# Performance work log

Hardware: AMD Instinct MI355X
Metric: run time of the kernel (lower is better)

The kernel has to match this reference:

```python
import jax, jax.numpy as jnp
import numpy as np

S, D = 16384, 1024


def setup_inputs() -> dict:
    key = jax.random.key(0)
    ks = jax.random.split(key, 7)
    stdv = 1.0 / np.sqrt(D)
    u = lambda k, shape: jax.random.uniform(k, shape, jnp.float32, -stdv, stdv)
    return {
        "x": jax.random.normal(ks[0], (S, D), jnp.float32),
        "Wq": u(ks[1], (D, D)), "bq": u(ks[2], (D,)),
        "Wk": u(ks[3], (D, D)), "bk": u(ks[4], (D,)),
        "Wv": u(ks[5], (D, D)), "bv": u(ks[6], (D,)),
    }


def reference(x, Wq, bq, Wk, bk, Wv, bv):
    # torch.nn.Linear: y = x @ W^T + b
    q = x @ Wq.T + bq          # [S, D]
    k = x @ Wk.T + bk          # [S, D]
    v = x @ Wv.T + bv          # [S, D]
    d = x.shape[-1]
    # NOTE: faithful to source -- scores are over the FEATURE axis: [D, D]
    scores = jnp.einsum('sd,se->de', q, k) / jnp.sqrt(jnp.float32(d))
    attn = jax.nn.softmax(scores, axis=-1)   # [D, D]
    out = v @ attn                           # [S, D]
    return out, attn
```

## Files before the change

### kernel.cpp

```cpp
#include <hip/hip_runtime.h>
#include <hip/hip_bf16.h>
#include <stdint.h>


#define S_ 16384
#define D_ 1024

typedef _Float16 half8 __attribute__((ext_vector_type(8)));
typedef _Float16 half4 __attribute__((ext_vector_type(4)));
typedef float f32x4 __attribute__((ext_vector_type(4)));

__device__ __forceinline__ void gload_lds16(const _Float16* g, _Float16* l) {
    __builtin_amdgcn_global_load_lds(
        (const __attribute__((address_space(1))) void*)g,
        (__attribute__((address_space(3))) void*)l, 16, 0, 0);
}

#define VM8() do { asm volatile("s_waitcnt vmcnt(8)" ::: "memory"); __builtin_amdgcn_sched_barrier(0); } while (0)
#define VM0() do { asm volatile("s_waitcnt vmcnt(0)" ::: "memory"); __builtin_amdgcn_sched_barrier(0); } while (0)
#define BAR() __builtin_amdgcn_s_barrier()
#define LGKM0() do { asm volatile("s_waitcnt lgkmcnt(0)" ::: "memory"); __builtin_amdgcn_sched_barrier(0); } while (0)
#define LGKM8() do { asm volatile("s_waitcnt lgkmcnt(8)" ::: "memory"); __builtin_amdgcn_sched_barrier(0); } while (0)
#define PRIO1() __builtin_amdgcn_s_setprio(1)
#define PRIO0() __builtin_amdgcn_s_setprio(0)

#define STAGEA(H, KT, NX) do { \
    const _Float16* _s = srcA + (size_t)((H) * 128) * lda + (size_t)(KT) * 64; \
    _Float16* _d = AsS + (NX) * 16384 + ((H) * 128 + 8 * w) * 64; \
    gload_lds16(_s, _d); \
    gload_lds16(_s + (size_t)64 * lda, _d + 4096); \
} while (0)

#define STAGEB(H, KT, NX) do { \
    const _Float16* _s = srcB + (size_t)((H) * 128) * ldb + (size_t)(KT) * 64; \
    _Float16* _d = BsS + (NX) * 16384 + ((H) * 128 + 8 * w) * 64; \
    gload_lds16(_s, _d); \
    gload_lds16(_s + (size_t)64 * ldb, _d + 4096); \
} while (0)

#define READA(PA, QA) do { _Pragma("unroll") \
    for (int fm = 0; fm < 4; ++fm) { \
        af[fm][0] = *(const half8*)((PA) + (((QA) * 128 + fm * 16) << 7) + cx0); \
        af[fm][1] = *(const half8*)((PA) + (((QA) * 128 + fm * 16) << 7) + cx1); } \
} while (0)

#define READB(PB, BF, QB) do { _Pragma("unroll") \
    for (int fn = 0; fn < 2; ++fn) { \
        BF[fn][0] = *(const half8*)((PB) + (((QB) * 128 + fn * 16) << 7) + cx0); \
        BF[fn][1] = *(const half8*)((PB) + (((QB) * 128 + fn * 16) << 7) + cx1); } \
} while (0)

#define MFMAB(QA, QB, BF) do { _Pragma("unroll") \
    for (int fm = 0; fm < 4; ++fm) { _Pragma("unroll") \
        for (int fn = 0; fn < 2; ++fn) { \
            f32x4 _c = acc[(QA) * 4 + fm][(QB) * 2 + fn]; \
            _c = __builtin_amdgcn_mfma_f32_16x16x32_f16(af[fm][0], BF[fn][0], _c, 0, 0, 0); \
            _c = __builtin_amdgcn_mfma_f32_16x16x32_f16(af[fm][1], BF[fn][1], _c, 0, 0, 0); \
            acc[(QA) * 4 + fm][(QB) * 2 + fn] = _c; } } \
} while (0)

__global__ __launch_bounds__(512, 2)
void gemm256(const _Float16* __restrict__ A, const _Float16* __restrict__ B,
             _Float16* __restrict__ C,
             int lda, int ldb, int ldc, int ksub, long long mn,
             int ntx, int ntxy, int cpx) {
    __shared__ _Float16 SM2[65536];
    _Float16* AsS = SM2;
    _Float16* BsS = SM2 + 32768;
    const int t = threadIdx.x;
    const int l = t & 63;
    const int w = t >> 6;
    const int wm = w >> 2, wn = w & 3;

    const int hb = blockIdx.x;
    const int lg = (hb & 7) * cpx + (hb >> 3);
    const int bz = lg / ntxy;
    const int rem = lg - bz * ntxy;
    const int by = rem / ntx;
    const int bx = rem - by * ntx;
    const size_t m0 = (size_t)by * 256;
    const size_t n0 = (size_t)bx * 256;
    const size_t k0 = (size_t)bz * (size_t)ksub;
    const long long coff = (long long)bz * mn;

    const int colsw = 8 * ((l & 7) ^ (l >> 3));
    const _Float16* srcA = A + (m0 + 8 * w + (l >> 3)) * (size_t)lda + k0 + colsw;
    const _Float16* srcB = B + (n0 + 8 * w + (l >> 3)) * (size_t)ldb + k0 + colsw;

    const int cx0 = (((l >> 4) << 4)) ^ ((l & 7) << 4);
    const int cx1 = (64 + ((l >> 4) << 4)) ^ ((l & 7) << 4);
    const char* basePA = (const char*)AsS + ((wm * 64 + (l & 15)) << 7);
    const char* basePB = (const char*)BsS + ((wn * 32 + (l & 15)) << 7);

    f32x4 acc[8][4] = {};
    half8 af[4][2], bf0[2][2], bf1[2][2];

    const int nk = ksub >> 6;

    STAGEA(0, 0, 0); STAGEB(0, 0, 0); STAGEB(1, 0, 0); STAGEA(1, 0, 0);
    STAGEA(0, 1, 1); STAGEB(0, 1, 1); STAGEB(1, 1, 1); STAGEA(1, 1, 1);

    for (int kt = 0; kt < nk; ++kt) {
        const int p = kt & 1;
        const int ks = kt + 2;
        const bool hs = ks < nk;
        const char* pA = basePA + p * 32768;
        const char* pB = basePB + p * 32768;

        if (kt == nk - 1) VM0(); else VM8();
        BAR();

        READA(pA, 0); READB(pB, bf0, 0);
        LGKM8();
        BAR(); LGKM0();
        PRIO1(); MFMAB(0, 0, bf0); PRIO0(); BAR();

        READB(pB, bf1, 1);
        if (hs) { STAGEA(0, ks, p); STAGEB(0, ks, p); }
        BAR(); LGKM0();
        PRIO1(); MFMAB(0, 1, bf1); PRIO0(); BAR();

        READA(pA, 1);
        if (hs) STAGEB(1, ks, p);
        BAR(); LGKM0();
        PRIO1(); MFMAB(1, 1, bf1); PRIO0(); BAR();

        if (hs) STAGEA(1, ks, p);
        PRIO1(); MFMAB(1, 0, bf0); PRIO0(); BAR();
    }

    _Float16* eb = SM2;
    const int cr = (l >> 4) << 2;
    const int cc = l & 15;
#pragma unroll
    for (int h = 0; h < 2; ++h) {
        BAR();
#pragma unroll
        for (int mm = 0; mm < 4; ++mm) {
#pragma unroll
            for (int n = 0; n < 4; ++n) {
                const int lrow0 = wm * 64 + mm * 16 + cr;
                const int lcol = (n >> 1) * 128 + wn * 32 + (n & 1) * 16 + cc;
#pragma unroll
                for (int r = 0; r < 4; ++r)
                    eb[(lrow0 + r) * 264 + lcol] = (_Float16)acc[h * 4 + mm][n][r];
            }
        }
        LGKM0();
        BAR();
#pragma unroll
        for (int i = 0; i < 8; ++i) {
            const int lrow = w * 16 + i * 2 + (l >> 5);
            const half8 v = *(const half8*)(eb + lrow * 264 + (l & 31) * 8);
            const size_t row = m0 + (size_t)h * 128 + lrow;
            const size_t col = n0 + (l & 31) * 8;
            __builtin_nontemporal_store(v,
                (half8*)(C + coff + (long long)row * ldc + col));
        }
        LGKM0();
    }
}

#define STG128(SRC, LD, DST, KT) do { \
    const _Float16* _s = (SRC) + (size_t)(KT) * 64; \
    _Float16* _d = (DST) + 8 * w * 64; \
    gload_lds16(_s, _d); \
    gload_lds16(_s + (size_t)32 * (LD), _d + 2048); \
    gload_lds16(_s + (size_t)64 * (LD), _d + 4096); \
    gload_lds16(_s + (size_t)96 * (LD), _d + 6144); \
} while (0)

__global__ __launch_bounds__(256, 2)
void gemm128(const _Float16* __restrict__ A, const _Float16* __restrict__ B,
             float* __restrict__ C, const float* __restrict__ bias,
             int lda, int ldb, int ldc, int ksub,
             int ntx, int cpx) {
    __shared__ _Float16 SM[32768];
    const int t = threadIdx.x;
    const int l = t & 63;
    const int w = t >> 6;
    const int wm = w >> 1, wn = w & 1;

    const int hb = blockIdx.x;
    const int lg = (hb & 7) * cpx + (hb >> 3);
    const int by = lg / ntx;
    const int bx = lg - by * ntx;
    const size_t m0 = (size_t)by * 128;
    const size_t n0 = (size_t)bx * 128;

    const int colsw = 8 * ((l & 7) ^ (l >> 3));
    const _Float16* srcA = A + (m0 + 8 * w + (l >> 3)) * (size_t)lda + colsw;
    const _Float16* srcB = B + (n0 + 8 * w + (l >> 3)) * (size_t)ldb + colsw;

    const int cx0 = (((l >> 4) << 4)) ^ ((l & 7) << 4);
    const int cx1 = (64 + ((l >> 4) << 4)) ^ ((l & 7) << 4);
    const char* basePA = (const char*)SM + ((wm * 64 + (l & 15)) << 7);
    const char* basePB = (const char*)SM + 32768 + ((wn * 64 + (l & 15)) << 7);

    f32x4 acc[4][4] = {};
    half8 af[4][2], bf[4][2];

    const int nk = ksub >> 6;

    STG128(srcA, lda, SM + 0, 0);        STG128(srcB, ldb, SM + 16384, 0);
    STG128(srcA, lda, SM + 8192, 1);     STG128(srcB, ldb, SM + 24576, 1);

    for (int kt = 0; kt < nk; ++kt) {
        const int p = kt & 1;
        const int ks = kt + 2;
        const bool hs = ks < nk;
        const char* pA = basePA + p * 16384;
        const char* pB = basePB + p * 16384;

        if (kt == nk - 1) VM0(); else VM8();
        BAR();

#pragma unroll
        for (int fm = 0; fm < 4; ++fm) {
            af[fm][0] = *(const half8*)(pA + ((fm * 16) << 7) + cx0);
            af[fm][1] = *(const half8*)(pA + ((fm * 16) << 7) + cx1);
        }
#pragma unroll
        for (int fn = 0; fn < 4; ++fn) {
            bf[fn][0] = *(const half8*)(pB + ((fn * 16) << 7) + cx0);
            bf[fn][1] = *(const half8*)(pB + ((fn * 16) << 7) + cx1);
        }
        LGKM0();
        PRIO1();
#pragma unroll
        for (int fm = 0; fm < 4; ++fm)
#pragma unroll
            for (int fn = 0; fn < 4; ++fn)
                acc[fm][fn] = __builtin_amdgcn_mfma_f32_16x16x32_f16(af[fm][0], bf[fn][0], acc[fm][fn], 0, 0, 0);
        PRIO0();
        BAR();

        if (hs) {
            STG128(srcA, lda, SM + p * 8192, ks);
            STG128(srcB, ldb, SM + 16384 + p * 8192, ks);
        }
        PRIO1();
#pragma unroll
        for (int fm = 0; fm < 4; ++fm)
#pragma unroll
            for (int fn = 0; fn < 4; ++fn)
                acc[fm][fn] = __builtin_amdgcn_mfma_f32_16x16x32_f16(af[fm][1], bf[fn][1], acc[fm][fn], 0, 0, 0);
        PRIO0();
        BAR();
    }

    float* lw = (float*)((char*)SM + w * 16384);
    const int cr = (l >> 4) << 2;
    const int cc = l & 15;
    float bb4[4];
#pragma unroll
    for (int fn = 0; fn < 4; ++fn)
        bb4[fn] = bias[n0 + wn * 64 + fn * 16 + cc];
#pragma unroll
    for (int h = 0; h < 2; ++h) {
#pragma unroll
        for (int mm2 = 0; mm2 < 2; ++mm2) {
            const int mm = h * 2 + mm2;
#pragma unroll
            for (int fn = 0; fn < 4; ++fn) {
                const int lcol = fn * 16 + cc;
                const int lrow = mm2 * 16 + cr;
#pragma unroll
                for (int r = 0; r < 4; ++r)
                    lw[(lrow + r) * 68 + lcol] = acc[mm][fn][r] + bb4[fn];
            }
        }
        LGKM0();
        const size_t grow0 = m0 + (size_t)wm * 64 + h * 32;
#pragma unroll
        for (int i = 0; i < 8; ++i) {
            const int lrow = i * 4 + (l >> 4);
            const int lcol = (l & 15) * 4;
            const f32x4 v = *(const f32x4*)(lw + lrow * 68 + lcol);
            __builtin_nontemporal_store(v,
                (f32x4*)(C + (size_t)(grow0 + lrow) * ldc + n0 + wn * 64 + lcol));
        }
        LGKM0();
    }
}

__global__ __launch_bounds__(256, 2)
void gemm_abt(const _Float16* __restrict__ A, const _Float16* __restrict__ B,
              float* __restrict__ C, int lda, int ldb, int ldc, int ksub,
              long long mn) {
    const int t = threadIdx.x;
    const int lane = t & 63;
    const int wave = t >> 6;
    const int wr = (wave >> 1) * 64;
    const int wc = (wave & 1) * 64;
    const size_t m0 = (size_t)blockIdx.y * 128;
    const size_t n0 = (size_t)blockIdx.x * 128;
    const size_t k0 = (size_t)blockIdx.z * (size_t)ksub;
    const long long coff = (long long)blockIdx.z * mn;

    __shared__ _Float16 As[128 * 32];
    __shared__ _Float16 Bs[128 * 32];

    f32x4 acc[4][4] = {};

    const _Float16* a0 = A + (m0 + (size_t)(t >> 2)) * (size_t)lda + k0 + (t & 3) * 8;
    const _Float16* a1 = a0 + (size_t)64 * lda;
    const _Float16* b0 = B + (n0 + (size_t)(t >> 2)) * (size_t)ldb + k0 + (t & 3) * 8;
    const _Float16* b1 = b0 + (size_t)64 * ldb;
    _Float16* AsW0 = As + wave * 512;
    _Float16* AsW1 = As + 2048 + wave * 512;
    _Float16* BsW0 = Bs + wave * 512;
    _Float16* BsW1 = Bs + 2048 + wave * 512;

    const int nk = ksub >> 5;
    for (int kt = 0; kt < nk; ++kt) {
        __syncthreads();
        gload_lds16(a0, AsW0);
        gload_lds16(a1, AsW1);
        gload_lds16(b0, BsW0);
        gload_lds16(b1, BsW1);
        a0 += 32; a1 += 32; b0 += 32; b1 += 32;
        __syncthreads();

        half8 af[4], bf[4];
#pragma unroll
        for (int i = 0; i < 4; ++i)
            af[i] = *(const half8*)(As + (wr + i * 16 + (lane & 15)) * 32 + (lane >> 4) * 8);
#pragma unroll
        for (int i = 0; i < 4; ++i)
            bf[i] = *(const half8*)(Bs + (wc + i * 16 + (lane & 15)) * 32 + (lane >> 4) * 8);
#pragma unroll
        for (int i = 0; i < 4; ++i)
#pragma unroll
            for (int j = 0; j < 4; ++j)
                acc[i][j] = __builtin_amdgcn_mfma_f32_16x16x32_f16(af[i], bf[j], acc[i][j], 0, 0, 0);
    }

    const int cr = (lane >> 4) * 4;
    const int cc = lane & 15;
#pragma unroll
    for (int i = 0; i < 4; ++i) {
#pragma unroll
        for (int j = 0; j < 4; ++j) {
            const size_t row0 = m0 + wr + i * 16 + cr;
            const size_t col = n0 + wc + j * 16 + cc;
#pragma unroll
            for (int r = 0; r < 4; ++r)
                C[coff + (long long)(row0 + r) * ldc + col] = acc[i][j][r];
        }
    }
}

template <int WRITE_ROW, int COLSUM>
__global__ __launch_bounds__(256)
void cast_transpose(const float* __restrict__ in, _Float16* __restrict__ outRow,
                    _Float16* __restrict__ outT, float* __restrict__ msum, int ldT) {
    __shared__ _Float16 tile[64][66];
    __shared__ float red[16][16][4];
    const int t = threadIdx.x;
    const int c0 = blockIdx.x * 64;
    const int r0 = blockIdx.y * 64;
    const int cg = t & 15;
    const int rb = t >> 4;
    f32x4 csum = {};
#pragma unroll
    for (int it = 0; it < 4; ++it) {
        const int rr = rb + it * 16;
        f32x4 v = *(const f32x4*)(in + (size_t)(r0 + rr) * 1024 + c0 + cg * 4);
        if (COLSUM) { csum[0] += v[0]; csum[1] += v[1]; csum[2] += v[2]; csum[3] += v[3]; }
        _Float16 h0 = (_Float16)v[0], h1 = (_Float16)v[1];
        _Float16 h2 = (_Float16)v[2], h3 = (_Float16)v[3];
        tile[rr][cg * 4 + 0] = h0; tile[rr][cg * 4 + 1] = h1;
        tile[rr][cg * 4 + 2] = h2; tile[rr][cg * 4 + 3] = h3;
        if (WRITE_ROW) {
            half4 h = {h0, h1, h2, h3};
            *(half4*)(outRow + (size_t)(r0 + rr) * 1024 + c0 + cg * 4) = h;
        }
    }
    if (COLSUM) {
        red[rb][cg][0] = csum[0]; red[rb][cg][1] = csum[1];
        red[rb][cg][2] = csum[2]; red[rb][cg][3] = csum[3];
    }
    __syncthreads();
    if (COLSUM && t < 64) {
        float s = 0.f;
#pragma unroll
        for (int k = 0; k < 16; ++k) s += red[k][t >> 2][t & 3];
        atomicAdd(msum + c0 + t, s);
    }
    const int i = t >> 2, ch = (t & 3) * 16;
    half8 h0v, h1v;
#pragma unroll
    for (int j = 0; j < 8; ++j) h0v[j] = tile[ch + j][i];
#pragma unroll
    for (int j = 0; j < 8; ++j) h1v[j] = tile[ch + 8 + j][i];
    *(half8*)(outT + (size_t)(c0 + i) * ldT + r0 + ch) = h0v;
    *(half8*)(outT + (size_t)(c0 + i) * ldT + r0 + ch + 8) = h1v;
}

__global__ __launch_bounds__(256)
void prep_w(const float* __restrict__ Wq, const float* __restrict__ Wk,
            const float* __restrict__ Wv, const float* __restrict__ bq,
            const float* __restrict__ m,
            _Float16* __restrict__ wq16, _Float16* __restrict__ wk16,
            _Float16* __restrict__ wvT16,
            float* __restrict__ u2, float* __restrict__ w) {
    __shared__ _Float16 tile[64][66];
    __shared__ float wred[4];
    const int b = blockIdx.x;
    const int t = threadIdx.x;

    if (b < 1024) {
        const bool isQ = b < 512;
        const int bb = isQ ? b : b - 512;
        const float* W = isQ ? Wq : Wk;
        _Float16* o = isQ ? wq16 : wk16;
        const size_t base = (size_t)bb * 2048 + (size_t)t * 8;
        const f32x4* p = (const f32x4*)(W + base);
        f32x4 x0 = p[0], x1 = p[1];
        half8 h;
        h[0] = (_Float16)x0[0]; h[1] = (_Float16)x0[1];
        h[2] = (_Float16)x0[2]; h[3] = (_Float16)x0[3];
        h[4] = (_Float16)x1[0]; h[5] = (_Float16)x1[1];
        h[6] = (_Float16)x1[2]; h[7] = (_Float16)x1[3];
        ((half8*)o)[bb * 256 + t] = h;
        const int col = (t * 8) & 1023;
        f32x4 m0 = *(const f32x4*)(m + col);
        f32x4 m1 = *(const f32x4*)(m + col + 4);
        float s = x0[0] * m0[0] + x0[1] * m0[1] + x0[2] * m0[2] + x0[3] * m0[3]
                + x1[0] * m1[0] + x1[1] * m1[1] + x1[2] * m1[2] + x1[3] * m1[3];
        for (int o2 = 32; o2; o2 >>= 1) s += __shfl_xor(s, o2);
        if ((t & 63) == 0) wred[t >> 6] = s;
        __syncthreads();
        if (t == 0) {
            const int rA = 2 * bb, rB = 2 * bb + 1;
            const float vA = wred[0] + wred[1];
            const float vB = wred[2] + wred[3];
            if (isQ) {
                u2[rA] = vA + 16384.0f * bq[rA];
                u2[rB] = vB + 16384.0f * bq[rB];
            } else {
                w[rA] = vA;
                w[rB] = vB;
            }
        }
        return;
    }

    const int bb = b - 1024;
    const int c0 = (bb & 15) * 64;
    const int r0 = (bb >> 4) * 64;
    const int cg = t & 15;
    const int rb = t >> 4;
#pragma unroll
    for (int it = 0; it < 4; ++it) {
        const int rr = rb + it * 16;
        f32x4 v = *(const f32x4*)(Wv + (size_t)(r0 + rr) * 1024 + c0 + cg * 4);
        tile[rr][cg * 4 + 0] = (_Float16)v[0];
        tile[rr][cg * 4 + 1] = (_Float16)v[1];
        tile[rr][cg * 4 + 2] = (_Float16)v[2];
        tile[rr][cg * 4 + 3] = (_Float16)v[3];
    }
    __syncthreads();
    const int i = t >> 2, ch = (t & 3) * 16;
    half8 h0v, h1v;
#pragma unroll
    for (int j = 0; j < 8; ++j) h0v[j] = tile[ch + j][i];
#pragma unroll
    for (int j = 0; j < 8; ++j) h1v[j] = tile[ch + 8 + j][i];
    *(half8*)(wvT16 + (size_t)(c0 + i) * 1024 + r0 + ch) = h0v;
    *(half8*)(wvT16 + (size_t)(c0 + i) * 1024 + r0 + ch + 8) = h1v;
}

__global__ void zero_vec(float* __restrict__ p, int n) {
    int i = blockIdx.x * 256 + threadIdx.x;
    if (i < n) p[i] = 0.f;
}

__global__ __launch_bounds__(256)
void reduce_g(const _Float16* __restrict__ part, _Float16* __restrict__ G16) {
    const size_t off = ((size_t)blockIdx.x * 256 + threadIdx.x) * 8;
    float s[8] = {};
    for (int z = 0; z < 16; ++z) {
        half8 v = *(const half8*)(part + (size_t)z * 1048576 + off);
#pragma unroll
        for (int j = 0; j < 8; ++j) s[j] += (float)v[j];
    }
    half8 o;
#pragma unroll
    for (int j = 0; j < 8; ++j) o[j] = (_Float16)s[j];
    *(half8*)(G16 + off) = o;
}

__global__ __launch_bounds__(256)
void reduce_cast(const float* __restrict__ part, _Float16* __restrict__ outh,
                 int nz, float scale) {
    const int idx = (blockIdx.x * 256 + threadIdx.x) * 4;
    f32x4 s = {};
    for (int z = 0; z < nz; ++z) {
        f32x4 v = *(const f32x4*)(part + (size_t)z * 1048576 + idx);
        s[0] += v[0]; s[1] += v[1]; s[2] += v[2]; s[3] += v[3];
    }
    half4 h;
    h[0] = (_Float16)(s[0] * scale); h[1] = (_Float16)(s[1] * scale);
    h[2] = (_Float16)(s[2] * scale); h[3] = (_Float16)(s[3] * scale);
    *(half4*)(outh + idx) = h;
}

__global__ __launch_bounds__(256)
void softmax_rows(const float* __restrict__ part, const float* __restrict__ u2,
                  const float* __restrict__ bq, const float* __restrict__ bk,
                  const float* __restrict__ w,
                  float* __restrict__ P, _Float16* __restrict__ PT) {
    const int a = blockIdx.x;
    const int t = threadIdx.x;
    __shared__ float red[8];
    const size_t off = (size_t)a * 1024 + t * 4;
    f32x4 s = {};
#pragma unroll
    for (int z = 0; z < 4; ++z) {
        f32x4 v = *(const f32x4*)(part + (size_t)z * 1048576 + off);
        s[0] += v[0]; s[1] += v[1]; s[2] += v[2]; s[3] += v[3];
    }
    const float ru = u2[a], rb = bq[a];
    f32x4 bk4 = *(const f32x4*)(bk + t * 4);
    f32x4 w4 = *(const f32x4*)(w + t * 4);
#pragma unroll
    for (int j = 0; j < 4; ++j) s[j] = (s[j] + ru * bk4[j] + rb * w4[j]) * 0.03125f;

    float m = fmaxf(fmaxf(s[0], s[1]), fmaxf(s[2], s[3]));
    for (int o = 32; o; o >>= 1) m = fmaxf(m, __shfl_xor(m, o));
    if ((t & 63) == 0) red[t >> 6] = m;
    __syncthreads();
    m = fmaxf(fmaxf(red[0], red[1]), fmaxf(red[2], red[3]));

    float e0 = expf(s[0] - m), e1 = expf(s[1] - m);
    float e2 = expf(s[2] - m), e3 = expf(s[3] - m);
    float sum = e0 + e1 + e2 + e3;
    for (int o = 32; o; o >>= 1) sum += __shfl_xor(sum, o);
    if ((t & 63) == 0) red[4 + (t >> 6)] = sum;
    __syncthreads();
    sum = red[4] + red[5] + red[6] + red[7];
    const float inv = 1.0f / sum;

    f32x4 o4 = {e0 * inv, e1 * inv, e2 * inv, e3 * inv};
    *(f32x4*)(P + off) = o4;
    const int b = t * 4;
    PT[(size_t)(b + 0) * 1024 + a] = (_Float16)o4[0];
    PT[(size_t)(b + 1) * 1024 + a] = (_Float16)o4[1];
    PT[(size_t)(b + 2) * 1024 + a] = (_Float16)o4[2];
    PT[(size_t)(b + 3) * 1024 + a] = (_Float16)o4[3];
}

__global__ __launch_bounds__(256)
void attn_bv(const float* __restrict__ attn, const float* __restrict__ bv,
             float* __restrict__ c) {
    const int j = blockIdx.x * 256 + threadIdx.x;
    const int a0 = blockIdx.y * 64;
    float s = 0.f;
#pragma unroll 4
    for (int k = 0; k < 64; ++k) {
        const int a = a0 + k;
        s += attn[(size_t)a * 1024 + j] * bv[a];
    }
    atomicAdd(c + j, s);
}

extern "C" void kernel_launch(void* const* d_in, const int* in_sizes, int n_in,
                              void* d_out, int out_size, void* d_ws, size_t ws_size,
                              hipStream_t stream) {
    const float* x  = (const float*)d_in[0];
    const float* Wq = (const float*)d_in[1];
    const float* bq = (const float*)d_in[2];
    const float* Wk = (const float*)d_in[3];
    const float* bk = (const float*)d_in[4];
    const float* Wv = (const float*)d_in[5];
    const float* bv = (const float*)d_in[6];
    float* out  = (float*)d_out;
    float* attn = out + (size_t)S_ * D_;

    char* ws = (char*)d_ws;
    float*    part  = (float*)ws;
    _Float16* partH = (_Float16*)ws;
    _Float16* x16   = (_Float16*)(ws + 33554432);
    _Float16* xT16  = (_Float16*)(ws + 67108864);
    _Float16* wq16  = (_Float16*)(ws + 100663296);
    _Float16* wk16  = (_Float16*)(ws + 102760448);
    _Float16* wvT16 = (_Float16*)(ws + 104857600);
    _Float16* G16   = (_Float16*)(ws + 106954752);
    _Float16* U16   = (_Float16*)(ws + 109051904);
    _Float16* PT    = (_Float16*)(ws + 111149056);
    _Float16* MT16  = (_Float16*)(ws + 113246208);
    float*    mvec  = (float*)(ws + 115343360);
    float*    u2    = mvec + 1024;
    float*    wv    = u2 + 1024;
    float*    cvec  = wv + 1024;

    zero_vec<<<16, 256, 0, stream>>>(mvec, 4096);
    cast_transpose<1, 1><<<dim3(16, 256), 256, 0, stream>>>(x, x16, xT16, mvec, S_);
    prep_w<<<1280, 256, 0, stream>>>(Wq, Wk, Wv, bq, mvec,
                                     wq16, wk16, wvT16, u2, wv);

    gemm256<<<256, 512, 0, stream>>>(xT16, xT16, partH,
                                     16384, 16384, 1024, 1024, 1048576LL,
                                     4, 16, 32);
    reduce_g<<<512, 256, 0, stream>>>(partH, G16);
    gemm_abt<<<dim3(8, 8, 4), 256, 0, stream>>>(wq16, G16, part,
                                                1024, 1024, 1024, 256, 1048576);
    reduce_cast<<<1024, 256, 0, stream>>>(part, U16, 4, 1.0f);
    gemm_abt<<<dim3(8, 8, 4), 256, 0, stream>>>(U16, wk16, part,
                                                1024, 1024, 1024, 256, 1048576);
    softmax_rows<<<1024, 256, 0, stream>>>(part, u2, bq, bk, wv, attn, PT);
    attn_bv<<<dim3(4, 16), 256, 0, stream>>>(attn, bv, cvec);
    gemm_abt<<<dim3(8, 8, 4), 256, 0, stream>>>(PT, wvT16, part,
                                                1024, 1024, 1024, 256, 1048576);
    reduce_cast<<<1024, 256, 0, stream>>>(part, MT16, 4, 1.0f);
    gemm128<<<1024, 256, 0, stream>>>(x16, MT16, out, cvec,
                                      1024, 1024, 1024, 1024, 8, 128);
}
```

Before: 183.0 us.

## Replace split-K 1024 GEMM with double-buffered swizzled LDS pipeline kernel

```diff
diff --git a/kernel.cpp b/kernel.cpp
--- a/kernel.cpp
+++ b/kernel.cpp
@@ -285,69 +285,108 @@
 }
 
 __global__ __launch_bounds__(256, 2)
-void gemm_abt(const _Float16* __restrict__ A, const _Float16* __restrict__ B,
-              float* __restrict__ C, int lda, int ldb, int ldc, int ksub,
-              long long mn) {
+void gemm_s128(const _Float16* __restrict__ A, const _Float16* __restrict__ B,
+               float* __restrict__ C, int lda, int ldb, int ldc, int ksub,
+               long long mn) {
+    __shared__ _Float16 SM[32768];
     const int t = threadIdx.x;
-    const int lane = t & 63;
-    const int wave = t >> 6;
-    const int wr = (wave >> 1) * 64;
-    const int wc = (wave & 1) * 64;
+    const int l = t & 63;
+    const int w = t >> 6;
+    const int wm = w >> 1, wn = w & 1;
+
     const size_t m0 = (size_t)blockIdx.y * 128;
     const size_t n0 = (size_t)blockIdx.x * 128;
     const size_t k0 = (size_t)blockIdx.z * (size_t)ksub;
     const long long coff = (long long)blockIdx.z * mn;
 
-    __shared__ _Float16 As[128 * 32];
-    __shared__ _Float16 Bs[128 * 32];
+    const int colsw = 8 * ((l & 7) ^ (l >> 3));
+    const _Float16* srcA = A + (m0 + 8 * w + (l >> 3)) * (size_t)lda + k0 + colsw;
+    const _Float16* srcB = B + (n0 + 8 * w + (l >> 3)) * (size_t)ldb + k0 + colsw;
+
+    const int cx0 = (((l >> 4) << 4)) ^ ((l & 7) << 4);
+    const int cx1 = (64 + ((l >> 4) << 4)) ^ ((l & 7) << 4);
+    const char* basePA = (const char*)SM + ((wm * 64 + (l & 15)) << 7);
+    const char* basePB = (const char*)SM + 32768 + ((wn * 64 + (l & 15)) << 7);
 
     f32x4 acc[4][4] = {};
-
-    const _Float16* a0 = A + (m0 + (size_t)(t >> 2)) * (size_t)lda + k0 + (t & 3) * 8;
-    const _Float16* a1 = a0 + (size_t)64 * lda;
-    const _Float16* b0 = B + (n0 + (size_t)(t >> 2)) * (size_t)ldb + k0 + (t & 3) * 8;
-    const _Float16* b1 = b0 + (size_t)64 * ldb;
-    _Float16* AsW0 = As + wave * 512;
-    _Float16* AsW1 = As + 2048 + wave * 512;
-    _Float16* BsW0 = Bs + wave * 512;
-    _Float16* BsW1 = Bs + 2048 + wave * 512;
-
-    const int nk = ksub >> 5;
+    half8 af[4][2], bf[4][2];
+
+    const int nk = ksub >> 6;
+
+    STG128(srcA, lda, SM + 0, 0);        STG128(srcB, ldb, SM + 16384, 0);
+    STG128(srcA, lda, SM + 8192, 1);     STG128(srcB, ldb, SM + 24576, 1);
+
     for (int kt = 0; kt < nk; ++kt) {
-        __syncthreads();
-        gload_lds16(a0, AsW0);
-        gload_lds16(a1, AsW1);
-        gload_lds16(b0, BsW0);
-        gload_lds16(b1, BsW1);
-        a0 += 32; a1 += 32; b0 += 32; b1 += 32;
-        __syncthreads();
-
-        half8 af[4], bf[4];
-#pragma unroll
-        for (int i = 0; i < 4; ++i)
-            af[i] = *(const half8*)(As + (wr + i * 16 + (lane & 15)) * 32 + (lane >> 4) * 8);
-#pragma unroll
-        for (int i = 0; i < 4; ++i)
-            bf[i] = *(const half8*)(Bs + (wc + i * 16 + (lane & 15)) * 32 + (lane >> 4) * 8);
-#pragma unroll
-        for (int i = 0; i < 4; ++i)
-#pragma unroll
-            for (int j = 0; j < 4; ++j)
-                acc[i][j] = __builtin_amdgcn_mfma_f32_16x16x32_f16(af[i], bf[j], acc[i][j], 0, 0, 0);
-    }
-
-    const int cr = (lane >> 4) * 4;
-    const int cc = lane & 15;
-#pragma unroll
-    for (int i = 0; i < 4; ++i) {
-#pragma unroll
-        for (int j = 0; j < 4; ++j) {
-            const size_t row0 = m0 + wr + i * 16 + cr;
-            const size_t col = n0 + wc + j * 16 + cc;
-#pragma unroll
-            for (int r = 0; r < 4; ++r)
-                C[coff + (long long)(row0 + r) * ldc + col] = acc[i][j][r];
-        }
+        const int p = kt & 1;
+        const int ks = kt + 2;
+        const bool hs = ks < nk;
+        const char* pA = basePA + p * 16384;
+        const char* pB = basePB + p * 16384;
+
+        if (kt == nk - 1) VM0(); else VM8();
+        BAR();
+
+#pragma unroll
+        for (int fm = 0; fm < 4; ++fm) {
+            af[fm][0] = *(const half8*)(pA + ((fm * 16) << 7) + cx0);
+            af[fm][1] = *(const half8*)(pA + ((fm * 16) << 7) + cx1);
+        }
+#pragma unroll
+        for (int fn = 0; fn < 4; ++fn) {
+            bf[fn][0] = *(const half8*)(pB + ((fn * 16) << 7) + cx0);
+            bf[fn][1] = *(const half8*)(pB + ((fn * 16) << 7) + cx1);
+        }
+        LGKM0();
+        PRIO1();
+#pragma unroll
+        for (int fm = 0; fm < 4; ++fm)
+#pragma unroll
+            for (int fn = 0; fn < 4; ++fn)
+                acc[fm][fn] = __builtin_amdgcn_mfma_f32_16x16x32_f16(af[fm][0], bf[fn][0], acc[fm][fn], 0, 0, 0);
+        PRIO0();
+        BAR();
+
+        if (hs) {
+            STG128(srcA, lda, SM + p * 8192, ks);
+            STG128(srcB, ldb, SM + 16384 + p * 8192, ks);
+        }
+        PRIO1();
+#pragma unroll
+        for (int fm = 0; fm < 4; ++fm)
+#pragma unroll
+            for (int fn = 0; fn < 4; ++fn)
+                acc[fm][fn] = __builtin_amdgcn_mfma_f32_16x16x32_f16(af[fm][1], bf[fn][1], acc[fm][fn], 0, 0, 0);
+        PRIO0();
+        BAR();
+    }
+
+    float* lw = (float*)((char*)SM + w * 16384);
+    const int cr = (l >> 4) << 2;
+    const int cc = l & 15;
+#pragma unroll
+    for (int h = 0; h < 2; ++h) {
+#pragma unroll
+        for (int mm2 = 0; mm2 < 2; ++mm2) {
+            const int mm = h * 2 + mm2;
+#pragma unroll
+            for (int fn = 0; fn < 4; ++fn) {
+                const int lcol = fn * 16 + cc;
+                const int lrow = mm2 * 16 + cr;
+#pragma unroll
+                for (int r = 0; r < 4; ++r)
+                    lw[(lrow + r) * 68 + lcol] = acc[mm][fn][r];
+            }
+        }
+        LGKM0();
+        const size_t grow0 = m0 + (size_t)wm * 64 + h * 32;
+#pragma unroll
+        for (int i = 0; i < 8; ++i) {
+            const int lrow = i * 4 + (l >> 4);
+            const int lcol = (l & 15) * 4;
+            const f32x4 v = *(const f32x4*)(lw + lrow * 68 + lcol);
+            *(f32x4*)(C + coff + (long long)(grow0 + lrow) * ldc + n0 + wn * 64 + lcol) = v;
+        }
+        LGKM0();
     }
 }
 
@@ -605,15 +644,15 @@
                                      16384, 16384, 1024, 1024, 1048576LL,
                                      4, 16, 32);
     reduce_g<<<512, 256, 0, stream>>>(partH, G16);
-    gemm_abt<<<dim3(8, 8, 4), 256, 0, stream>>>(wq16, G16, part,
-                                                1024, 1024, 1024, 256, 1048576);
+    gemm_s128<<<dim3(8, 8, 4), 256, 0, stream>>>(wq16, G16, part,
+                                                 1024, 1024, 1024, 256, 1048576);
     reduce_cast<<<1024, 256, 0, stream>>>(part, U16, 4, 1.0f);
-    gemm_abt<<<dim3(8, 8, 4), 256, 0, stream>>>(U16, wk16, part,
-                                                1024, 1024, 1024, 256, 1048576);
+    gemm_s128<<<dim3(8, 8, 4), 256, 0, stream>>>(U16, wk16, part,
+                                                 1024, 1024, 1024, 256, 1048576);
     softmax_rows<<<1024, 256, 0, stream>>>(part, u2, bq, bk, wv, attn, PT);
     attn_bv<<<dim3(4, 16), 256, 0, stream>>>(attn, bv, cvec);
-    gemm_abt<<<dim3(8, 8, 4), 256, 0, stream>>>(PT, wvT16, part,
-                                                1024, 1024, 1024, 256, 1048576);
+    gemm_s128<<<dim3(8, 8, 4), 256, 0, stream>>>(PT, wvT16, part,
+                                                 1024, 1024, 1024, 256, 1048576);
     reduce_cast<<<1024, 256, 0, stream>>>(part, MT16, 4, 1.0f);
     gemm128<<<1024, 256, 0, stream>>>(x16, MT16, out, cvec,
                                       1024, 1024, 1024, 1024, 8, 128);
```

Measured after the change: 177.2 us. 1.03x faster.
